# Kernel optimization log

Measured on AMD Instinct MI355X. Metric: run time of the kernel, lower is better.

Reference implementation:

```python
import jax, jax.numpy as jnp
from jax import lax
import numpy as np

B, SQ, SK, H, NH, KS = 2, 2048, 2048, 1024, 16, 3
D = H // NH  # depth per head = 64


def setup_inputs() -> dict:
    key = jax.random.key(0)
    ks = jax.random.split(key, 10)
    s = 0.02
    return {
        "query_input": jax.random.normal(ks[0], (B, SQ, H), jnp.float32),
        "source_input": jax.random.normal(ks[1], (B, SK, H), jnp.float32),
        "mask": jnp.zeros((B, 1, 1, SK), jnp.float32),
        "Wq": jax.random.normal(ks[2], (KS, H, H), jnp.float32) * s,
        "bq": jnp.zeros((H,), jnp.float32),
        "Wk": jax.random.normal(ks[3], (KS, H, H), jnp.float32) * s,
        "bk": jnp.zeros((H,), jnp.float32),
        "Wv": jax.random.normal(ks[4], (KS, H, H), jnp.float32) * s,
        "bv": jnp.zeros((H,), jnp.float32),
        "Wo": jax.random.normal(ks[5], (H, H), jnp.float32) * s,
        "bo": jnp.zeros((H,), jnp.float32),
    }


def _conv1d_same(x, W, b):
    # x: [B, S, H], W: [KS, H_in, H_out] -> 'same' padded 1D conv
    y = lax.conv_general_dilated(x, W, window_strides=(1,), padding="SAME",
                                 dimension_numbers=("NWC", "WIO", "NWC"))
    return y + b


def _split_heads(x):
    # [B, S, H] -> [B, NH, S, D]
    b, s, _ = x.shape
    return x.reshape(b, s, NH, D).transpose(0, 2, 1, 3)


def reference(query_input, source_input, mask, Wq, bq, Wk, bk, Wv, bv, Wo, bo):
    q = _split_heads(_conv1d_same(query_input, Wq, bq)) * (D ** -0.5)
    k = _split_heads(_conv1d_same(source_input, Wk, bk))
    v = _split_heads(_conv1d_same(source_input, Wv, bv))
    logits = jnp.einsum("bhqd,bhkd->bhqk", q, k) + mask * (-1e9)
    weights = jax.nn.softmax(logits, axis=-1)  # dropout omitted (eval mode)
    attn = jnp.einsum("bhqk,bhkd->bhqd", weights, v)
    attn = attn.transpose(0, 2, 1, 3).reshape(q.shape[0], -1, H)
    return attn @ Wo + bo
```

## Files before the change

### kernel.cpp

```cpp
#include <hip/hip_runtime.h>
#include <stdint.h>

#define B_   2
#define S_   2048
#define H_   1024
#define NH_  16
#define D_   64
#define KC_  3072

typedef __attribute__((ext_vector_type(8))) short  short8;
typedef __attribute__((ext_vector_type(4))) float  floatx4;

typedef __attribute__((address_space(1))) const void gas_void;
typedef __attribute__((address_space(3))) void       las_void;

__device__ __forceinline__ void gld16(const void* g, void* l) {
    __builtin_amdgcn_global_load_lds((gas_void*)g, (las_void*)l, 16, 0, 0);
}

__device__ __forceinline__ unsigned short f2bf(float f) {
    union { float f; unsigned u; } v; v.f = f;
    unsigned r = v.u + 0x7fffu + ((v.u >> 16) & 1u);
    return (unsigned short)(r >> 16);
}

__global__ __launch_bounds__(256) void k_pad_convert(const float* __restrict__ src,
                                                     unsigned short* __restrict__ dst) {
    int gid = blockIdx.x * 256 + threadIdx.x;
    int vid = gid * 4;
    if (vid >= B_ * 2050 * 1024) return;
    int row = vid >> 10;
    int b   = (row >= 2050) ? 1 : 0;
    int r   = row - b * 2050;
    int h   = vid & 1023;
    unsigned short o0 = 0, o1 = 0, o2 = 0, o3 = 0;
    if (r != 0 && r != 2049) {
        const float4 f = *(const float4*)(src + ((b * 2048 + r - 1) << 10) + h);
        o0 = f2bf(f.x); o1 = f2bf(f.y); o2 = f2bf(f.z); o3 = f2bf(f.w);
    }
    ushort4 o; o.x = o0; o.y = o1; o.z = o2; o.w = o3;
    *(ushort4*)(dst + vid) = o;
}

__global__ void k_transpose_bf16(const float* __restrict__ src,
                                 unsigned short* __restrict__ dst, int R, int C) {
    __shared__ float t[32][33];
    int c0 = blockIdx.x * 32, r0 = blockIdx.y * 32;
    int tx = threadIdx.x, ty = threadIdx.y;
#pragma unroll
    for (int k = 0; k < 4; ++k)
        t[ty + k * 8][tx] = src[(long)(r0 + ty + k * 8) * C + c0 + tx];
    __syncthreads();
#pragma unroll
    for (int k = 0; k < 4; ++k)
        dst[(long)(c0 + ty + k * 8) * R + r0 + tx] = f2bf(t[tx][ty + k * 8]);
}

__global__ __launch_bounds__(256) void k_conv_gemm(
    const unsigned short* __restrict__ xq, const unsigned short* __restrict__ xs,
    const unsigned short* __restrict__ Wqt, const unsigned short* __restrict__ Wkt,
    const unsigned short* __restrict__ Wvt,
    const float* __restrict__ bq, const float* __restrict__ bk, const float* __restrict__ bv,
    unsigned short* __restrict__ Qo, unsigned short* __restrict__ Ko,
    unsigned short* __restrict__ Vo) {
    int z = blockIdx.z;
    const unsigned short* X = (z == 0) ? xq : xs;
    const unsigned short* W = (z == 0) ? Wqt : (z == 1 ? Wkt : Wvt);
    const float* bias = (z == 0) ? bq : (z == 1 ? bk : bv);

    __shared__ unsigned short Al[128 * 64];
    __shared__ unsigned short Bl[128 * 64];

    int n0 = blockIdx.x * 128, m0 = blockIdx.y * 128;
    int b = m0 >> 11;
    int tid = threadIdx.x, lane = tid & 63, w = tid >> 6;
    int quad = lane >> 4, l15 = lane & 15;
    int wm = w >> 1, wn = w & 1;

    floatx4 acc[4][4];
#pragma unroll
    for (int i = 0; i < 4; ++i)
#pragma unroll
        for (int j = 0; j < 4; ++j) acc[i][j] = (floatx4){0.f, 0.f, 0.f, 0.f};

    int arow0 = (m0 + 2 * b) * 1024;

    for (int k0 = 0; k0 < KC_; k0 += 64) {
#pragma unroll
        for (int it = 0; it < 4; ++it) {
            int e  = (it * 256 + tid) * 8;
            int rl = e >> 6;
            int cp = (e >> 3) & 7;
            int c  = cp ^ (rl & 7);
            gld16(X + arow0 + rl * 1024 + k0 + c * 8, (char*)Al + e * 2);
            gld16(W + (n0 + rl) * KC_ + k0 + c * 8, (char*)Bl + e * 2);
        }
        __syncthreads();
#pragma unroll
        for (int kk = 0; kk < 2; ++kk) {
            short8 af[4], bf[4];
#pragma unroll
            for (int i = 0; i < 4; ++i) {
                int m  = wm * 64 + i * 16 + l15;
                int cp = (kk * 4 + quad) ^ (m & 7);
                af[i]  = *(const short8*)(Al + m * 64 + cp * 8);
            }
#pragma unroll
            for (int j = 0; j < 4; ++j) {
                int n  = wn * 64 + j * 16 + l15;
                int cp = (kk * 4 + quad) ^ (n & 7);
                bf[j]  = *(const short8*)(Bl + n * 64 + cp * 8);
            }
#pragma unroll
            for (int i = 0; i < 4; ++i)
#pragma unroll
                for (int j = 0; j < 4; ++j)
                    acc[i][j] = __builtin_amdgcn_mfma_f32_16x16x32_bf16(af[i], bf[j], acc[i][j], 0, 0, 0);
        }
        __syncthreads();
    }

#pragma unroll
    for (int j = 0; j < 4; ++j) {
        int n = n0 + wn * 64 + j * 16 + l15;
        float bb = bias[n];
        int nh = n >> 6, d = n & 63;
#pragma unroll
        for (int i = 0; i < 4; ++i) {
            int srow = (m0 & 2047) + wm * 64 + i * 16 + quad * 4;
#pragma unroll
            for (int r = 0; r < 4; ++r) {
                float v = acc[i][j][r] + bb;
                int s = srow + r;
                if (z == 0)
                    Qo[((b * NH_ + nh) * 2048 + s) * 64 + d] = f2bf(v * 0.125f);
                else if (z == 1)
                    Ko[((b * NH_ + nh) * 2048 + s) * 64 + d] = f2bf(v);
                else
                    Vo[((b * NH_ + nh) * 64 + d) * 2048 + s] = f2bf(v);
            }
        }
    }
}

__global__ __launch_bounds__(256) void k_flash(
    const unsigned short* __restrict__ Q, const unsigned short* __restrict__ K,
    const unsigned short* __restrict__ Vt, const float* __restrict__ mask,
    unsigned short* __restrict__ Ao) {
    __shared__ unsigned short Ul[128 * 136];
    __shared__ unsigned short Vl[64 * 128];

    int tid = threadIdx.x, w = tid >> 6, lane = tid & 63;
    int quad = lane >> 4, l15 = lane & 15;
    int bh = blockIdx.y;
    int b = bh >> 4, nh = bh & 15;
    int q0 = blockIdx.x * 128, wq = w * 32;

    short8 qf[2][2];
#pragma unroll
    for (int i = 0; i < 2; ++i)
#pragma unroll
        for (int kk = 0; kk < 2; ++kk)
            qf[i][kk] = *(const short8*)(Q + ((bh * 2048 + q0 + wq + i * 16 + l15) << 6) + kk * 32 + quad * 8);

    floatx4 oacc[2][4];
    float rsum[2][4];
#pragma unroll
    for (int i = 0; i < 2; ++i) {
#pragma unroll
        for (int j = 0; j < 4; ++j) oacc[i][j] = (floatx4){0.f, 0.f, 0.f, 0.f};
#pragma unroll
        for (int r = 0; r < 4; ++r) rsum[i][r] = 0.f;
    }
    const float* maskb = mask + b * S_;

    for (int kt = 0; kt < 16; ++kt) {
        int k0 = kt * 128;
#pragma unroll
        for (int it = 0; it < 4; ++it) {
            int e  = (it * 256 + tid) * 8;
            int kl = e >> 6;
            int c  = ((e >> 3) & 7) ^ (kl & 7);
            gld16(K + (bh * 2048 + k0 + kl) * 64 + c * 8, (char*)Ul + e * 2);
            int dl = e >> 7;
            int cp = (e >> 3) & 15;
            int c2 = (cp & 8) | ((cp ^ dl) & 7);
            gld16(Vt + (bh * 64 + dl) * 2048 + k0 + c2 * 8, (char*)Vl + e * 2);
        }
        __syncthreads();

        floatx4 sacc[2][8];
#pragma unroll
        for (int i = 0; i < 2; ++i)
#pragma unroll
            for (int j = 0; j < 8; ++j) sacc[i][j] = (floatx4){0.f, 0.f, 0.f, 0.f};
#pragma unroll
        for (int j = 0; j < 8; ++j) {
            int kl = j * 16 + l15;
            short8 bf0, bf1;
            {
                int cp = (0 * 4 + quad) ^ (kl & 7);
                bf0 = *(const short8*)(Ul + kl * 64 + cp * 8);
                int cq = (1 * 4 + quad) ^ (kl & 7);
                bf1 = *(const short8*)(Ul + kl * 64 + cq * 8);
            }
#pragma unroll
            for (int i = 0; i < 2; ++i) {
                sacc[i][j] = __builtin_amdgcn_mfma_f32_16x16x32_bf16(qf[i][0], bf0, sacc[i][j], 0, 0, 0);
                sacc[i][j] = __builtin_amdgcn_mfma_f32_16x16x32_bf16(qf[i][1], bf1, sacc[i][j], 0, 0, 0);
            }
        }
        __syncthreads();

#pragma unroll
        for (int j = 0; j < 8; ++j) {
            float mv = maskb[k0 + j * 16 + l15] * (-1e9f);
#pragma unroll
            for (int i = 0; i < 2; ++i) {
                int row = wq + i * 16 + quad * 4;
#pragma unroll
                for (int r = 0; r < 4; ++r) {
                    float p = __expf(sacc[i][j][r] + mv);
                    rsum[i][r] += p;
                    Ul[(row + r) * 136 + j * 16 + l15] = f2bf(p);
                }
            }
        }

#pragma unroll
        for (int kk = 0; kk < 4; ++kk) {
            short8 af[2], bv4[4];
#pragma unroll
            for (int i = 0; i < 2; ++i)
                af[i] = *(const short8*)(Ul + (wq + i * 16 + l15) * 136 + kk * 32 + quad * 8);
#pragma unroll
            for (int j2 = 0; j2 < 4; ++j2) {
                int dl = j2 * 16 + l15;
                int c  = kk * 4 + quad;
                int cp = (c & 8) | ((c ^ dl) & 7);
                bv4[j2] = *(const short8*)(Vl + dl * 128 + cp * 8);
            }
#pragma unroll
            for (int i = 0; i < 2; ++i)
#pragma unroll
                for (int j2 = 0; j2 < 4; ++j2)
                    oacc[i][j2] = __builtin_amdgcn_mfma_f32_16x16x32_bf16(af[i], bv4[j2], oacc[i][j2], 0, 0, 0);
        }
        __syncthreads();
    }

#pragma unroll
    for (int i = 0; i < 2; ++i)
#pragma unroll
        for (int r = 0; r < 4; ++r) {
            float v = rsum[i][r];
            v += __shfl_xor(v, 1); v += __shfl_xor(v, 2);
            v += __shfl_xor(v, 4); v += __shfl_xor(v, 8);
            rsum[i][r] = 1.0f / v;
        }

#pragma unroll
    for (int i = 0; i < 2; ++i)
#pragma unroll
        for (int j2 = 0; j2 < 4; ++j2)
#pragma unroll
            for (int r = 0; r < 4; ++r) {
                int qrow = q0 + wq + i * 16 + quad * 4 + r;
                int hcol = nh * 64 + j2 * 16 + l15;
                Ao[(b * 2048 + qrow) * 1024 + hcol] = f2bf(oacc[i][j2][r] * rsum[i][r]);
            }
}

__global__ __launch_bounds__(256) void k_proj_gemm(
    const unsigned short* __restrict__ A, const unsigned short* __restrict__ Wt,
    const float* __restrict__ bo, float* __restrict__ out) {
    __shared__ unsigned short Al[128 * 64];
    __shared__ unsigned short Bl[128 * 64];

    int n0 = blockIdx.x * 128, m0 = blockIdx.y * 128;
    int tid = threadIdx.x, lane = tid & 63, w = tid >> 6;
    int quad = lane >> 4, l15 = lane & 15;
    int wm = w >> 1, wn = w & 1;

    floatx4 acc[4][4];
#pragma unroll
    for (int i = 0; i < 4; ++i)
#pragma unroll
        for (int j = 0; j < 4; ++j) acc[i][j] = (floatx4){0.f, 0.f, 0.f, 0.f};

    for (int k0 = 0; k0 < 1024; k0 += 64) {
#pragma unroll
        for (int it = 0; it < 4; ++it) {
            int e  = (it * 256 + tid) * 8;
            int rl = e >> 6;
            int cp = (e >> 3) & 7;
            int c  = cp ^ (rl & 7);
            gld16(A + (m0 + rl) * 1024 + k0 + c * 8, (char*)Al + e * 2);
            gld16(Wt + (n0 + rl) * 1024 + k0 + c * 8, (char*)Bl + e * 2);
        }
        __syncthreads();
#pragma unroll
        for (int kk = 0; kk < 2; ++kk) {
            short8 af[4], bf[4];
#pragma unroll
            for (int i = 0; i < 4; ++i) {
                int m  = wm * 64 + i * 16 + l15;
                int cp = (kk * 4 + quad) ^ (m & 7);
                af[i]  = *(const short8*)(Al + m * 64 + cp * 8);
            }
#pragma unroll
            for (int j = 0; j < 4; ++j) {
                int n  = wn * 64 + j * 16 + l15;
                int cp = (kk * 4 + quad) ^ (n & 7);
                bf[j]  = *(const short8*)(Bl + n * 64 + cp * 8);
            }
#pragma unroll
            for (int i = 0; i < 4; ++i)
#pragma unroll
                for (int j = 0; j < 4; ++j)
                    acc[i][j] = __builtin_amdgcn_mfma_f32_16x16x32_bf16(af[i], bf[j], acc[i][j], 0, 0, 0);
        }
        __syncthreads();
    }

#pragma unroll
    for (int j = 0; j < 4; ++j) {
        int n = n0 + wn * 64 + j * 16 + l15;
        float bb = bo[n];
#pragma unroll
        for (int i = 0; i < 4; ++i) {
            int m = m0 + wm * 64 + i * 16 + quad * 4;
#pragma unroll
            for (int r = 0; r < 4; ++r)
                out[(m + r) * 1024 + n] = acc[i][j][r] + bb;
        }
    }
}

extern "C" void kernel_launch(void* const* d_in, const int* in_sizes, int n_in,
                              void* d_out, int out_size, void* d_ws, size_t ws_size,
                              hipStream_t stream) {
    (void)in_sizes; (void)n_in; (void)out_size; (void)ws_size;
    const float* q_in = (const float*)d_in[0];
    const float* s_in = (const float*)d_in[1];
    const float* mask = (const float*)d_in[2];
    const float* Wq   = (const float*)d_in[3];
    const float* bq   = (const float*)d_in[4];
    const float* Wk   = (const float*)d_in[5];
    const float* bk   = (const float*)d_in[6];
    const float* Wv   = (const float*)d_in[7];
    const float* bv   = (const float*)d_in[8];
    const float* Wo   = (const float*)d_in[9];
    const float* bo   = (const float*)d_in[10];
    float* out = (float*)d_out;

    char* ws = (char*)d_ws;
    size_t off = 0;
    auto alloc = [&](size_t bytes) {
        char* p = ws + off;
        off += (bytes + 255) & ~(size_t)255;
        return p;
    };
    unsigned short* xqp = (unsigned short*)alloc((size_t)B_ * 2050 * 1024 * 2);
    unsigned short* xsp = (unsigned short*)alloc((size_t)B_ * 2050 * 1024 * 2);
    unsigned short* Wqt = (unsigned short*)alloc((size_t)KC_ * H_ * 2);
    unsigned short* Wkt = (unsigned short*)alloc((size_t)KC_ * H_ * 2);
    unsigned short* Wvt = (unsigned short*)alloc((size_t)KC_ * H_ * 2);
    unsigned short* Wot = (unsigned short*)alloc((size_t)H_ * H_ * 2);
    unsigned short* Qb  = (unsigned short*)alloc((size_t)B_ * NH_ * S_ * D_ * 2);
    unsigned short* Kb  = (unsigned short*)alloc((size_t)B_ * NH_ * S_ * D_ * 2);
    unsigned short* Vtb = (unsigned short*)alloc((size_t)B_ * NH_ * S_ * D_ * 2);
    unsigned short* Ab  = (unsigned short*)alloc((size_t)B_ * S_ * H_ * 2);

    k_pad_convert<<<4100, 256, 0, stream>>>(q_in, xqp);
    k_pad_convert<<<4100, 256, 0, stream>>>(s_in, xsp);
    k_transpose_bf16<<<dim3(32, 96), dim3(32, 8), 0, stream>>>(Wq, Wqt, KC_, H_);
    k_transpose_bf16<<<dim3(32, 96), dim3(32, 8), 0, stream>>>(Wk, Wkt, KC_, H_);
    k_transpose_bf16<<<dim3(32, 96), dim3(32, 8), 0, stream>>>(Wv, Wvt, KC_, H_);
    k_transpose_bf16<<<dim3(32, 32), dim3(32, 8), 0, stream>>>(Wo, Wot, H_, H_);
    k_conv_gemm<<<dim3(8, 32, 3), 256, 0, stream>>>(xqp, xsp, Wqt, Wkt, Wvt,
                                                    bq, bk, bv, Qb, Kb, Vtb);
    k_flash<<<dim3(16, 32), 256, 0, stream>>>(Qb, Kb, Vtb, mask, Ab);
    k_proj_gemm<<<dim3(8, 32), 256, 0, stream>>>(Ab, Wot, bo, out);
}
```

Baseline: 358.1 us.

## Register-prefetch GEMM/flash tiles, widen flash blocks, halve proj GEMM M-tile

All three GEMM-style kernels drop the direct global-to-LDS loads. They now load the next k-tile into registers right after the barrier and store it to LDS at the top of the next iteration, so global latency overlaps the MFMA work. The flash kernel moves to 512 threads with 16 query rows per wave instead of 32, which halves per-wave registers and raises wave count. The output projection uses 64-row M tiles to double the grid from 256 to 512 blocks. The costs are extra VGPRs for the staging buffers and lower per-wave MFMA reuse of the K/V tiles in flash.

```diff
diff --git a/kernel.cpp b/kernel.cpp
--- a/kernel.cpp
+++ b/kernel.cpp
@@ -10,13 +10,6 @@
 
 typedef __attribute__((ext_vector_type(8))) short  short8;
 typedef __attribute__((ext_vector_type(4))) float  floatx4;
-
-typedef __attribute__((address_space(1))) const void gas_void;
-typedef __attribute__((address_space(3))) void       las_void;
-
-__device__ __forceinline__ void gld16(const void* g, void* l) {
-    __builtin_amdgcn_global_load_lds((gas_void*)g, (las_void*)l, 16, 0, 0);
-}
 
 __device__ __forceinline__ unsigned short f2bf(float f) {
     union { float f; unsigned u; } v; v.f = f;
@@ -85,17 +78,40 @@
 
     int arow0 = (m0 + 2 * b) * 1024;
 
-    for (int k0 = 0; k0 < KC_; k0 += 64) {
+    int eoff[4], aoff[4], boff[4];
+#pragma unroll
+    for (int it = 0; it < 4; ++it) {
+        int e  = (it * 256 + tid) * 8;
+        int rl = e >> 6;
+        int cp = (e >> 3) & 7;
+        int c  = cp ^ (rl & 7);
+        eoff[it] = e;
+        aoff[it] = arow0 + rl * 1024 + c * 8;
+        boff[it] = (n0 + rl) * KC_ + c * 8;
+    }
+
+    int4 ra[4], rb[4];
+#pragma unroll
+    for (int it = 0; it < 4; ++it) {
+        ra[it] = *(const int4*)(X + aoff[it]);
+        rb[it] = *(const int4*)(W + boff[it]);
+    }
+
+    for (int kt = 0; kt < 48; ++kt) {
 #pragma unroll
         for (int it = 0; it < 4; ++it) {
-            int e  = (it * 256 + tid) * 8;
-            int rl = e >> 6;
-            int cp = (e >> 3) & 7;
-            int c  = cp ^ (rl & 7);
-            gld16(X + arow0 + rl * 1024 + k0 + c * 8, (char*)Al + e * 2);
-            gld16(W + (n0 + rl) * KC_ + k0 + c * 8, (char*)Bl + e * 2);
-        }
-        __syncthreads();
+            *(int4*)((char*)Al + eoff[it] * 2) = ra[it];
+            *(int4*)((char*)Bl + eoff[it] * 2) = rb[it];
+        }
+        __syncthreads();
+        if (kt + 1 < 48) {
+            int k0 = (kt + 1) * 64;
+#pragma unroll
+            for (int it = 0; it < 4; ++it) {
+                ra[it] = *(const int4*)(X + aoff[it] + k0);
+                rb[it] = *(const int4*)(W + boff[it] + k0);
+            }
+        }
 #pragma unroll
         for (int kk = 0; kk < 2; ++kk) {
             short8 af[4], bf[4];
@@ -143,7 +159,7 @@
     }
 }
 
-__global__ __launch_bounds__(256) void k_flash(
+__global__ __launch_bounds__(512) void k_flash(
     const unsigned short* __restrict__ Q, const unsigned short* __restrict__ K,
     const unsigned short* __restrict__ Vt, const float* __restrict__ mask,
     unsigned short* __restrict__ Ao) {
@@ -154,85 +170,90 @@
     int quad = lane >> 4, l15 = lane & 15;
     int bh = blockIdx.y;
     int b = bh >> 4, nh = bh & 15;
-    int q0 = blockIdx.x * 128, wq = w * 32;
-
-    short8 qf[2][2];
-#pragma unroll
-    for (int i = 0; i < 2; ++i)
-#pragma unroll
-        for (int kk = 0; kk < 2; ++kk)
-            qf[i][kk] = *(const short8*)(Q + ((bh * 2048 + q0 + wq + i * 16 + l15) << 6) + kk * 32 + quad * 8);
-
-    floatx4 oacc[2][4];
-    float rsum[2][4];
-#pragma unroll
-    for (int i = 0; i < 2; ++i) {
-#pragma unroll
-        for (int j = 0; j < 4; ++j) oacc[i][j] = (floatx4){0.f, 0.f, 0.f, 0.f};
-#pragma unroll
-        for (int r = 0; r < 4; ++r) rsum[i][r] = 0.f;
-    }
+    int q0 = blockIdx.x * 128, wq = w * 16;
+
+    short8 qf[2];
+#pragma unroll
+    for (int kk = 0; kk < 2; ++kk)
+        qf[kk] = *(const short8*)(Q + ((bh * 2048 + q0 + wq + l15) << 6) + kk * 32 + quad * 8);
+
+    floatx4 oacc[4];
+    float rsum[4];
+#pragma unroll
+    for (int j = 0; j < 4; ++j) oacc[j] = (floatx4){0.f, 0.f, 0.f, 0.f};
+#pragma unroll
+    for (int r = 0; r < 4; ++r) rsum[r] = 0.f;
     const float* maskb = mask + b * S_;
+
+    int ek[2], kof[2], vof[2];
+#pragma unroll
+    for (int it = 0; it < 2; ++it) {
+        int e  = (it * 512 + tid) * 8;
+        ek[it] = e;
+        int kl = e >> 6;
+        int c  = ((e >> 3) & 7) ^ (kl & 7);
+        kof[it] = (bh * 2048 + kl) * 64 + c * 8;
+        int dl = e >> 7;
+        int cp = (e >> 3) & 15;
+        int c2 = (cp & 8) | ((cp ^ dl) & 7);
+        vof[it] = (bh * 64 + dl) * 2048 + c2 * 8;
+    }
+
+    int4 rk[2], rv[2];
+#pragma unroll
+    for (int it = 0; it < 2; ++it) {
+        rk[it] = *(const int4*)(K + kof[it]);
+        rv[it] = *(const int4*)(Vt + vof[it]);
+    }
 
     for (int kt = 0; kt < 16; ++kt) {
         int k0 = kt * 128;
 #pragma unroll
-        for (int it = 0; it < 4; ++it) {
-            int e  = (it * 256 + tid) * 8;
-            int kl = e >> 6;
-            int c  = ((e >> 3) & 7) ^ (kl & 7);
-            gld16(K + (bh * 2048 + k0 + kl) * 64 + c * 8, (char*)Ul + e * 2);
-            int dl = e >> 7;
-            int cp = (e >> 3) & 15;
-            int c2 = (cp & 8) | ((cp ^ dl) & 7);
-            gld16(Vt + (bh * 64 + dl) * 2048 + k0 + c2 * 8, (char*)Vl + e * 2);
-        }
-        __syncthreads();
-
-        floatx4 sacc[2][8];
-#pragma unroll
-        for (int i = 0; i < 2; ++i)
-#pragma unroll
-            for (int j = 0; j < 8; ++j) sacc[i][j] = (floatx4){0.f, 0.f, 0.f, 0.f};
+        for (int it = 0; it < 2; ++it) {
+            *(int4*)((char*)Ul + ek[it] * 2) = rk[it];
+            *(int4*)((char*)Vl + ek[it] * 2) = rv[it];
+        }
+        __syncthreads();
+        if (kt < 15) {
+            int kn = (kt + 1) * 128;
+#pragma unroll
+            for (int it = 0; it < 2; ++it) {
+                rk[it] = *(const int4*)(K + kof[it] + kn * 64);
+                rv[it] = *(const int4*)(Vt + vof[it] + kn);
+            }
+        }
+
+        floatx4 sacc[8];
+#pragma unroll
+        for (int j = 0; j < 8; ++j) sacc[j] = (floatx4){0.f, 0.f, 0.f, 0.f};
 #pragma unroll
         for (int j = 0; j < 8; ++j) {
             int kl = j * 16 + l15;
-            short8 bf0, bf1;
-            {
-                int cp = (0 * 4 + quad) ^ (kl & 7);
-                bf0 = *(const short8*)(Ul + kl * 64 + cp * 8);
-                int cq = (1 * 4 + quad) ^ (kl & 7);
-                bf1 = *(const short8*)(Ul + kl * 64 + cq * 8);
-            }
-#pragma unroll
-            for (int i = 0; i < 2; ++i) {
-                sacc[i][j] = __builtin_amdgcn_mfma_f32_16x16x32_bf16(qf[i][0], bf0, sacc[i][j], 0, 0, 0);
-                sacc[i][j] = __builtin_amdgcn_mfma_f32_16x16x32_bf16(qf[i][1], bf1, sacc[i][j], 0, 0, 0);
-            }
+            int cp0 = (0 * 4 + quad) ^ (kl & 7);
+            short8 bf0 = *(const short8*)(Ul + kl * 64 + cp0 * 8);
+            int cp1 = (1 * 4 + quad) ^ (kl & 7);
+            short8 bf1 = *(const short8*)(Ul + kl * 64 + cp1 * 8);
+            sacc[j] = __builtin_amdgcn_mfma_f32_16x16x32_bf16(qf[0], bf0, sacc[j], 0, 0, 0);
+            sacc[j] = __builtin_amdgcn_mfma_f32_16x16x32_bf16(qf[1], bf1, sacc[j], 0, 0, 0);
         }
         __syncthreads();
 
 #pragma unroll
         for (int j = 0; j < 8; ++j) {
             float mv = maskb[k0 + j * 16 + l15] * (-1e9f);
-#pragma unroll
-            for (int i = 0; i < 2; ++i) {
-                int row = wq + i * 16 + quad * 4;
-#pragma unroll
-                for (int r = 0; r < 4; ++r) {
-                    float p = __expf(sacc[i][j][r] + mv);
-                    rsum[i][r] += p;
-                    Ul[(row + r) * 136 + j * 16 + l15] = f2bf(p);
-                }
+            int row = wq + quad * 4;
+#pragma unroll
+            for (int r = 0; r < 4; ++r) {
+                float p = __expf(sacc[j][r] + mv);
+                rsum[r] += p;
+                Ul[(row + r) * 136 + j * 16 + l15] = f2bf(p);
             }
         }
 
 #pragma unroll
         for (int kk = 0; kk < 4; ++kk) {
-            short8 af[2], bv4[4];
-#pragma unroll
-            for (int i = 0; i < 2; ++i)
-                af[i] = *(const short8*)(Ul + (wq + i * 16 + l15) * 136 + kk * 32 + quad * 8);
+            short8 af = *(const short8*)(Ul + (wq + l15) * 136 + kk * 32 + quad * 8);
+            short8 bv4[4];
 #pragma unroll
             for (int j2 = 0; j2 < 4; ++j2) {
                 int dl = j2 * 16 + l15;
@@ -241,70 +262,90 @@
                 bv4[j2] = *(const short8*)(Vl + dl * 128 + cp * 8);
             }
 #pragma unroll
-            for (int i = 0; i < 2; ++i)
-#pragma unroll
-                for (int j2 = 0; j2 < 4; ++j2)
-                    oacc[i][j2] = __builtin_amdgcn_mfma_f32_16x16x32_bf16(af[i], bv4[j2], oacc[i][j2], 0, 0, 0);
-        }
-        __syncthreads();
-    }
-
-#pragma unroll
-    for (int i = 0; i < 2; ++i)
+            for (int j2 = 0; j2 < 4; ++j2)
+                oacc[j2] = __builtin_amdgcn_mfma_f32_16x16x32_bf16(af, bv4[j2], oacc[j2], 0, 0, 0);
+        }
+        __syncthreads();
+    }
+
+#pragma unroll
+    for (int r = 0; r < 4; ++r) {
+        float v = rsum[r];
+        v += __shfl_xor(v, 1); v += __shfl_xor(v, 2);
+        v += __shfl_xor(v, 4); v += __shfl_xor(v, 8);
+        rsum[r] = 1.0f / v;
+    }
+
+#pragma unroll
+    for (int j2 = 0; j2 < 4; ++j2)
 #pragma unroll
         for (int r = 0; r < 4; ++r) {
-            float v = rsum[i][r];
-            v += __shfl_xor(v, 1); v += __shfl_xor(v, 2);
-            v += __shfl_xor(v, 4); v += __shfl_xor(v, 8);
-            rsum[i][r] = 1.0f / v;
-        }
-
-#pragma unroll
-    for (int i = 0; i < 2; ++i)
-#pragma unroll
-        for (int j2 = 0; j2 < 4; ++j2)
-#pragma unroll
-            for (int r = 0; r < 4; ++r) {
-                int qrow = q0 + wq + i * 16 + quad * 4 + r;
-                int hcol = nh * 64 + j2 * 16 + l15;
-                Ao[(b * 2048 + qrow) * 1024 + hcol] = f2bf(oacc[i][j2][r] * rsum[i][r]);
-            }
+            int qrow = q0 + wq + quad * 4 + r;
+            int hcol = nh * 64 + j2 * 16 + l15;
+            Ao[(b * 2048 + qrow) * 1024 + hcol] = f2bf(oacc[j2][r] * rsum[r]);
+        }
 }
 
 __global__ __launch_bounds__(256) void k_proj_gemm(
     const unsigned short* __restrict__ A, const unsigned short* __restrict__ Wt,
     const float* __restrict__ bo, float* __restrict__ out) {
-    __shared__ unsigned short Al[128 * 64];
+    __shared__ unsigned short Al[64 * 64];
     __shared__ unsigned short Bl[128 * 64];
 
-    int n0 = blockIdx.x * 128, m0 = blockIdx.y * 128;
+    int n0 = blockIdx.x * 128, m0 = blockIdx.y * 64;
     int tid = threadIdx.x, lane = tid & 63, w = tid >> 6;
     int quad = lane >> 4, l15 = lane & 15;
     int wm = w >> 1, wn = w & 1;
 
-    floatx4 acc[4][4];
-#pragma unroll
-    for (int i = 0; i < 4; ++i)
+    floatx4 acc[2][4];
+#pragma unroll
+    for (int i = 0; i < 2; ++i)
 #pragma unroll
         for (int j = 0; j < 4; ++j) acc[i][j] = (floatx4){0.f, 0.f, 0.f, 0.f};
 
-    for (int k0 = 0; k0 < 1024; k0 += 64) {
-#pragma unroll
-        for (int it = 0; it < 4; ++it) {
-            int e  = (it * 256 + tid) * 8;
-            int rl = e >> 6;
-            int cp = (e >> 3) & 7;
-            int c  = cp ^ (rl & 7);
-            gld16(A + (m0 + rl) * 1024 + k0 + c * 8, (char*)Al + e * 2);
-            gld16(Wt + (n0 + rl) * 1024 + k0 + c * 8, (char*)Bl + e * 2);
-        }
-        __syncthreads();
+    int ea[2], ao[2], eb[4], bo_[4];
+#pragma unroll
+    for (int it = 0; it < 2; ++it) {
+        int e  = (it * 256 + tid) * 8;
+        int rl = e >> 6;
+        int c  = ((e >> 3) & 7) ^ (rl & 7);
+        ea[it] = e;
+        ao[it] = (m0 + rl) * 1024 + c * 8;
+    }
+#pragma unroll
+    for (int it = 0; it < 4; ++it) {
+        int e  = (it * 256 + tid) * 8;
+        int rl = e >> 6;
+        int c  = ((e >> 3) & 7) ^ (rl & 7);
+        eb[it] = e;
+        bo_[it] = (n0 + rl) * 1024 + c * 8;
+    }
+
+    int4 ra[2], rb[4];
+#pragma unroll
+    for (int it = 0; it < 2; ++it) ra[it] = *(const int4*)(A + ao[it]);
+#pragma unroll
+    for (int it = 0; it < 4; ++it) rb[it] = *(const int4*)(Wt + bo_[it]);
+
+    for (int kt = 0; kt < 16; ++kt) {
+#pragma unroll
+        for (int it = 0; it < 2; ++it) *(int4*)((char*)Al + ea[it] * 2) = ra[it];
+#pragma unroll
+        for (int it = 0; it < 4; ++it) *(int4*)((char*)Bl + eb[it] * 2) = rb[it];
+        __syncthreads();
+        if (kt + 1 < 16) {
+            int k0 = (kt + 1) * 64;
+#pragma unroll
+            for (int it = 0; it < 2; ++it) ra[it] = *(const int4*)(A + ao[it] + k0);
+#pragma unroll
+            for (int it = 0; it < 4; ++it) rb[it] = *(const int4*)(Wt + bo_[it] + k0);
+        }
 #pragma unroll
         for (int kk = 0; kk < 2; ++kk) {
-            short8 af[4], bf[4];
-#pragma unroll
-            for (int i = 0; i < 4; ++i) {
-                int m  = wm * 64 + i * 16 + l15;
+            short8 af[2], bf[4];
+#pragma unroll
+            for (int i = 0; i < 2; ++i) {
+                int m  = wm * 32 + i * 16 + l15;
                 int cp = (kk * 4 + quad) ^ (m & 7);
                 af[i]  = *(const short8*)(Al + m * 64 + cp * 8);
             }
@@ -315,7 +356,7 @@
                 bf[j]  = *(const short8*)(Bl + n * 64 + cp * 8);
             }
 #pragma unroll
-            for (int i = 0; i < 4; ++i)
+            for (int i = 0; i < 2; ++i)
 #pragma unroll
                 for (int j = 0; j < 4; ++j)
                     acc[i][j] = __builtin_amdgcn_mfma_f32_16x16x32_bf16(af[i], bf[j], acc[i][j], 0, 0, 0);
@@ -328,8 +369,8 @@
         int n = n0 + wn * 64 + j * 16 + l15;
         float bb = bo[n];
 #pragma unroll
-        for (int i = 0; i < 4; ++i) {
-            int m = m0 + wm * 64 + i * 16 + quad * 4;
+        for (int i = 0; i < 2; ++i) {
+            int m = m0 + wm * 32 + i * 16 + quad * 4;
 #pragma unroll
             for (int r = 0; r < 4; ++r)
                 out[(m + r) * 1024 + n] = acc[i][j][r] + bb;
@@ -380,6 +421,6 @@
     k_transpose_bf16<<<dim3(32, 32), dim3(32, 8), 0, stream>>>(Wo, Wot, H_, H_);
     k_conv_gemm<<<dim3(8, 32, 3), 256, 0, stream>>>(xqp, xsp, Wqt, Wkt, Wvt,
                                                     bq, bk, bv, Qb, Kb, Vtb);
-    k_flash<<<dim3(16, 32), 256, 0, stream>>>(Qb, Kb, Vtb, mask, Ab);
-    k_proj_gemm<<<dim3(8, 32), 256, 0, stream>>>(Ab, Wot, bo, out);
-}
+    k_flash<<<dim3(16, 32), 512, 0, stream>>>(Qb, Kb, Vtb, mask, Ab);
+    k_proj_gemm<<<dim3(8, 64), 256, 0, stream>>>(Ab, Wot, bo, out);
+}
```

New measurement: 664.0 us. 1.85x slower.
